# Optimization experiments

Hardware: AMD Instinct MI355X
Metric: run time of the kernel (lower is better)

## Reference

```python
import jax, jax.numpy as jnp
import numpy as np

VAR = 1.0
STD = float(np.sqrt(VAR))


def setup_inputs() -> dict:
    key = jax.random.key(0)
    k1, k2 = jax.random.split(key)
    n, c = 262144, 100
    scores = jax.random.normal(k1, (n, c), dtype=jnp.float32)
    labels = jax.random.randint(k2, (n,), 0, c, dtype=jnp.int64)
    return {"scores": scores, "labels": labels}


def reference(scores, labels):
    n, c = scores.shape
    # Gaussian pdf over class indices, centered at each label (re_encode_label)
    x = jnp.arange(c, dtype=scores.dtype)[None, :]            # (1, c)
    mu = labels.astype(scores.dtype)[:, None]                  # (n, 1)
    inv_norm = 1.0 / (STD * np.sqrt(2.0 * np.pi))
    code = inv_norm * jnp.exp(-0.5 * ((x - mu) / STD) ** 2)    # (n, c)
    # target distribution: softmax over the (unnormalized) pdf values
    target = jax.nn.softmax(code, axis=1)
    logsfmx = jax.nn.log_softmax(scores, axis=1)
    # KLDivLoss(reduction='batchmean'): sum(target * (log target - input)) / n
    kl = jnp.sum(target * (jnp.log(target) - logsfmx)) / n
    return kl
```

## Files before the change

### kernel.cpp

```cpp
#include <hip/hip_runtime.h>
#include <math.h>

#define C 100
#define INV_NORM 0.3989422804014327f
#define WFAR     0.67102943f

__device__ __constant__ float WP_dev[8] = {
    0.32897057f, 0.18369895f, 0.03722540f, 0.00298049f,
    8.9804e-5f,  9.9763e-7f,  4.0768e-9f,  0.f };

__device__ __forceinline__ float quad_sum(float x) {
    x += __int_as_float(__builtin_amdgcn_update_dpp(
            0, __float_as_int(x), 0xB1, 0xF, 0xF, true));
    x += __int_as_float(__builtin_amdgcn_update_dpp(
            0, __float_as_int(x), 0x4E, 0xF, 0xF, true));
    return x;
}

__global__ __launch_bounds__(256) void kl_main(
    const float* __restrict__ scores,
    const int*   __restrict__ labels,
    float* __restrict__ out, int n, float inv_n)
{
    __shared__ float wq[16];
    __shared__ float wpart[4];

    const int tid = threadIdx.x;
    if (tid < 16) wq[tid] = (tid < 8) ? WP_dev[tid] : 0.f;
    __syncthreads();

    const int wave = tid >> 6, lane = tid & 63;
    const int r = lane >> 2, sub = lane & 3;
    const int myrow = blockIdx.x * 64 + wave * 16 + r;

    float acc = 0.f;
    if (myrow < n) {
        const float4* rp4 = (const float4*)(scores + (size_t)myrow * C);
        const int mu = labels[myrow];

        float4 v[6];
        #pragma unroll
        for (int c = 0; c < 6; ++c) v[c] = rp4[sub + 4 * c];
        float4 v6 = make_float4(0.f, 0.f, 0.f, 0.f);
        if (sub == 0) v6 = rp4[24];

        const int bf = min(max(mu - 6, 0) >> 2, 21);
        const float4 wv = rp4[bf + sub];

        float se = 0.f, rs = 0.f;
        #pragma unroll
        for (int c = 0; c < 6; ++c) {
            se += __expf(v[c].x) + __expf(v[c].y) + __expf(v[c].z) + __expf(v[c].w);
            rs += v[c].x + v[c].y + v[c].z + v[c].w;
        }
        if (sub == 0) {
            se += __expf(v6.x) + __expf(v6.y) + __expf(v6.z) + __expf(v6.w);
            rs += v6.x + v6.y + v6.z + v6.w;
        }

        float p = 0.f;
        {
            const int jb = 4 * (bf + sub);
            const float el[4] = {wv.x, wv.y, wv.z, wv.w};
            #pragma unroll
            for (int cmp = 0; cmp < 4; ++cmp) {
                int d = jb + cmp - mu;
                int a = d < 0 ? -d : d;
                p = fmaf(wq[a], el[cmp], p);
            }
        }
        p = fmaf(WFAR, rs, p);

        se = quad_sum(se);
        p  = quad_sum(p);

        if (sub == 0) {
            constexpr float WPc[7] = {0.32897057f, 0.18369895f, 0.03722540f,
                0.00298049f, 8.9804e-5f, 9.9763e-7f, 4.0768e-9f};
            constexpr float WCc[7] = {0.39894228f, 0.20681926f, 0.03823936f,
                0.00298711f, 8.9816e-5f, 9.9765e-7f, 4.0768e-9f};
            float csum = 100.f * WFAR, dotc = 0.f;
            #pragma unroll
            for (int k = 0; k < 13; ++k) {
                const int d = k - 6, a = d < 0 ? -d : d;
                const bool ok = (unsigned)(mu + d) < (unsigned)C;
                csum += ok ? WPc[a] : 0.f;
                dotc += ok ? WCc[a] : 0.f;
            }
            const float rcs = __builtin_amdgcn_rcpf(csum);
            acc = fmaf(dotc - p, rcs, __logf(se) - __logf(csum)) - INV_NORM;
        }
    }

    #pragma unroll
    for (int off = 32; off > 0; off >>= 1)
        acc += __shfl_xor(acc, off, 64);
    if (lane == 0) wpart[wave] = acc;
    __syncthreads();
    if (tid == 0)
        atomicAdd(out, (wpart[0] + wpart[1] + wpart[2] + wpart[3]) * inv_n);
}

extern "C" void kernel_launch(void* const* d_in, const int* in_sizes, int n_in,
                              void* d_out, int out_size, void* d_ws, size_t ws_size,
                              hipStream_t stream)
{
    const float* scores = (const float*)d_in[0];
    const int*   labels = (const int*)d_in[1];
    float*       out    = (float*)d_out;

    int n = in_sizes[0] / C;

    hipMemsetAsync(d_out, 0, sizeof(float) * (size_t)out_size, stream);

    int blocks = (n + 63) / 64;
    kl_main<<<blocks, 256, 0, stream>>>(scores, labels, out, n, 1.0f / (float)n);
}
```

Baseline: 175.8 us.

## Map each row to a 32-lane half-wave with one float4 per lane

```diff
diff --git a/kernel.cpp b/kernel.cpp
--- a/kernel.cpp
+++ b/kernel.cpp
@@ -2,93 +2,100 @@
 #include <math.h>
 
 #define C 100
+#define PAIRS 8
+#define PASSES 2
+#define ROWS_PER_WAVE  (2 * PAIRS * PASSES)
+#define ROWS_PER_BLOCK (4 * ROWS_PER_WAVE)
 #define INV_NORM 0.3989422804014327f
 #define WFAR     0.67102943f
 
-__device__ __constant__ float WP_dev[8] = {
-    0.32897057f, 0.18369895f, 0.03722540f, 0.00298049f,
-    8.9804e-5f,  9.9763e-7f,  4.0768e-9f,  0.f };
+__device__ __constant__ float WPc[7] = {0.32897057f, 0.18369895f, 0.03722540f,
+    0.00298049f, 8.9804e-5f, 9.9763e-7f, 4.0768e-9f};
+__device__ __constant__ float WCc[7] = {0.39894228f, 0.20681926f, 0.03823936f,
+    0.00298711f, 8.9816e-5f, 9.9765e-7f, 4.0768e-9f};
 
-__device__ __forceinline__ float quad_sum(float x) {
-    x += __int_as_float(__builtin_amdgcn_update_dpp(
-            0, __float_as_int(x), 0xB1, 0xF, 0xF, true));
-    x += __int_as_float(__builtin_amdgcn_update_dpp(
-            0, __float_as_int(x), 0x4E, 0xF, 0xF, true));
+template <int CTRL>
+__device__ __forceinline__ float dpp_add(float x) {
+    return x + __int_as_float(__builtin_amdgcn_update_dpp(
+        0, __float_as_int(x), CTRL, 0xF, 0xF, true));
+}
+__device__ __forceinline__ float group32_sum(float x) {
+    x = dpp_add<0xB1>(x);
+    x = dpp_add<0x4E>(x);
+    x = dpp_add<0x118>(x);
+    x = dpp_add<0x114>(x);
+    x = dpp_add<0x142>(x);
     return x;
 }
 
-__global__ __launch_bounds__(256) void kl_main(
+__global__ __launch_bounds__(256, 6) void kl_main(
     const float* __restrict__ scores,
     const int*   __restrict__ labels,
     float* __restrict__ out, int n, float inv_n)
 {
-    __shared__ float wq[16];
+    __shared__ float Ktab[C], Rtab[C], wq[16];
     __shared__ float wpart[4];
 
     const int tid = threadIdx.x;
-    if (tid < 16) wq[tid] = (tid < 8) ? WP_dev[tid] : 0.f;
+    if (tid < C) {
+        float csum = (float)C * WFAR, dotc = 0.f;
+        #pragma unroll
+        for (int d = -6; d <= 6; ++d) {
+            bool ok = (unsigned)(tid + d) < (unsigned)C;
+            int a = d < 0 ? -d : d;
+            csum += ok ? WPc[a] : 0.f;
+            dotc += ok ? WCc[a] : 0.f;
+        }
+        Rtab[tid] = 1.0f / csum;
+        Ktab[tid] = dotc / csum - INV_NORM - __logf(csum);
+    }
+    if (tid < 16) wq[tid] = (tid < 7) ? WPc[tid] : 0.f;
     __syncthreads();
 
     const int wave = tid >> 6, lane = tid & 63;
-    const int r = lane >> 2, sub = lane & 3;
-    const int myrow = blockIdx.x * 64 + wave * 16 + r;
+    const int sub  = lane & 31;
+    const int half = lane >> 5;
+    const int waveRow0 = blockIdx.x * ROWS_PER_BLOCK + wave * ROWS_PER_WAVE;
+    const float4* g4 = (const float4*)scores;
 
     float acc = 0.f;
-    if (myrow < n) {
-        const float4* rp4 = (const float4*)(scores + (size_t)myrow * C);
-        const int mu = labels[myrow];
 
-        float4 v[6];
+    for (int pass = 0; pass < PASSES; ++pass) {
+        const int base = waveRow0 + pass * (2 * PAIRS);
+
+        float4 v[PAIRS]; int mu[PAIRS];
         #pragma unroll
-        for (int c = 0; c < 6; ++c) v[c] = rp4[sub + 4 * c];
-        float4 v6 = make_float4(0.f, 0.f, 0.f, 0.f);
-        if (sub == 0) v6 = rp4[24];
-
-        const int bf = min(max(mu - 6, 0) >> 2, 21);
-        const float4 wv = rp4[bf + sub];
-
-        float se = 0.f, rs = 0.f;
-        #pragma unroll
-        for (int c = 0; c < 6; ++c) {
-            se += __expf(v[c].x) + __expf(v[c].y) + __expf(v[c].z) + __expf(v[c].w);
-            rs += v[c].x + v[c].y + v[c].z + v[c].w;
-        }
-        if (sub == 0) {
-            se += __expf(v6.x) + __expf(v6.y) + __expf(v6.z) + __expf(v6.w);
-            rs += v6.x + v6.y + v6.z + v6.w;
+        for (int p = 0; p < PAIRS; ++p) {
+            int row = base + 2 * p + half;
+            bool ok = (sub < 25) && (row < n);
+            v[p]  = ok ? g4[(size_t)row * 25 + sub]
+                       : make_float4(0.f, 0.f, 0.f, 0.f);
+            mu[p] = (row < n) ? labels[row] : 0;
         }
 
-        float p = 0.f;
-        {
-            const int jb = 4 * (bf + sub);
-            const float el[4] = {wv.x, wv.y, wv.z, wv.w};
+        #pragma unroll
+        for (int p = 0; p < PAIRS; ++p) {
+            float se = __expf(v[p].x) + __expf(v[p].y)
+                     + __expf(v[p].z) + __expf(v[p].w);
+            float rs = v[p].x + v[p].y + v[p].z + v[p].w;
+
+            const int jb = 4 * sub;
+            const float el[4] = {v[p].x, v[p].y, v[p].z, v[p].w};
+            float dotw = 0.f;
             #pragma unroll
             for (int cmp = 0; cmp < 4; ++cmp) {
-                int d = jb + cmp - mu;
-                int a = d < 0 ? -d : d;
-                p = fmaf(wq[a], el[cmp], p);
+                int d = jb + cmp - mu[p];
+                int a = min(d < 0 ? -d : d, 15);
+                dotw = fmaf(wq[a], el[cmp], dotw);
             }
-        }
-        p = fmaf(WFAR, rs, p);
+            float q = fmaf(WFAR, rs, dotw);
 
-        se = quad_sum(se);
-        p  = quad_sum(p);
+            float seR = group32_sum(se);
+            float qR  = group32_sum(q);
 
-        if (sub == 0) {
-            constexpr float WPc[7] = {0.32897057f, 0.18369895f, 0.03722540f,
-                0.00298049f, 8.9804e-5f, 9.9763e-7f, 4.0768e-9f};
-            constexpr float WCc[7] = {0.39894228f, 0.20681926f, 0.03823936f,
-                0.00298711f, 8.9816e-5f, 9.9765e-7f, 4.0768e-9f};
-            float csum = 100.f * WFAR, dotc = 0.f;
-            #pragma unroll
-            for (int k = 0; k < 13; ++k) {
-                const int d = k - 6, a = d < 0 ? -d : d;
-                const bool ok = (unsigned)(mu + d) < (unsigned)C;
-                csum += ok ? WPc[a] : 0.f;
-                dotc += ok ? WCc[a] : 0.f;
-            }
-            const float rcs = __builtin_amdgcn_rcpf(csum);
-            acc = fmaf(dotc - p, rcs, __logf(se) - __logf(csum)) - INV_NORM;
+            int row = base + 2 * p + half;
+            if ((lane == 28 || lane == 60) && row < n)
+                acc += Ktab[mu[p]] + __logf(seR - 28.f) - Rtab[mu[p]] * qR;
         }
     }
 
@@ -111,8 +118,8 @@
 
     int n = in_sizes[0] / C;
 
-    hipMemsetAsync(d_out, 0, sizeof(float) * (size_t)out_size, stream);
+    (void)hipMemsetAsync(d_out, 0, sizeof(float) * (size_t)out_size, stream);
 
-    int blocks = (n + 63) / 64;
+    int blocks = (n + ROWS_PER_BLOCK - 1) / ROWS_PER_BLOCK;
     kl_main<<<blocks, 256, 0, stream>>>(scores, labels, out, n, 1.0f / (float)n);
 }
```

Result: faster. 163.0 us (-7.3%).
